# Kernel optimization log

Measured on AMD Instinct MI355X. Metric: run time of the kernel, lower is better.

The kernel has to match this reference:

```python
import jax, jax.numpy as jnp
import numpy as np

N_NODES = 50000
N_EDGES = 400000
NODE_DIM = 128
NUM_BASIS = 20
MUL0, MUL1, MUL2 = 128, 64, 32          # 128x0e + 64x1e + 32x2e
NUM_IRREPS = MUL0 + MUL1 + MUL2         # 224
SPH_DIM = MUL0 + 3 * MUL1 + 5 * MUL2    # 480
HIDDEN = NODE_DIM + NUM_IRREPS          # 352
EPS = 1e-5


def layer_norm(x, g, b):
    mu = x.mean(-1, keepdims=True)
    var = ((x - mu) ** 2).mean(-1, keepdims=True)
    return (x - mu) * jax.lax.rsqrt(var + EPS) * g + b


def o3_layer_norm(x, w, b):
    # Equivariant layer norm per irrep block (Equiformer-style, component normalization).
    s = x[:, :MUL0]                                    # l=0 scalars [N,128]
    v = x[:, MUL0:MUL0 + 3 * MUL1].reshape(-1, MUL1, 3)  # l=1 [N,64,3]
    t = x[:, MUL0 + 3 * MUL1:].reshape(-1, MUL2, 5)      # l=2 [N,32,5]
    s = s - s.mean(-1, keepdims=True)
    s = s * jax.lax.rsqrt((s ** 2).mean(-1, keepdims=True) + EPS) * w[:MUL0] + b
    nv = (v ** 2).mean(axis=(-1, -2))[:, None, None]
    v = v * jax.lax.rsqrt(nv + EPS) * w[MUL0:MUL0 + MUL1][None, :, None]
    nt = (t ** 2).mean(axis=(-1, -2))[:, None, None]
    t = t * jax.lax.rsqrt(nt + EPS) * w[MUL0 + MUL1:][None, :, None]
    return jnp.concatenate([s, v.reshape(-1, 3 * MUL1), t.reshape(-1, 5 * MUL2)], axis=-1)


def sph_harm(vec):
    # e3nn spherical harmonics (normalize=True, normalization='component') up to l=2.
    u = vec * jax.lax.rsqrt((vec ** 2).sum(-1, keepdims=True))
    x, y, z = u[:, 0], u[:, 1], u[:, 2]
    s15 = np.float32(np.sqrt(15.0))
    s5 = np.float32(np.sqrt(5.0))
    sh1 = np.float32(np.sqrt(3.0)) * u  # [E,3]
    sh2 = jnp.stack([s15 * x * z,
                     s15 * x * y,
                     s5 * (y * y - 0.5 * (x * x + z * z)),
                     s15 * y * z,
                     0.5 * s15 * (z * z - x * x)], axis=-1)  # [E,5]
    return sh1, sh2


def _forward(x_scalar, x_spherical, rbf, vec, W1, b1, W2, b2, Wrbf, ln_g, ln_b, o3_w, o3_b, edge_index):
    dst, src = edge_index[0], edge_index[1]
    scalar_in = layer_norm(x_scalar, ln_g, ln_b)          # [N,128]
    spherical_in = o3_layer_norm(x_spherical, o3_w, o3_b)  # [N,480]
    h = jax.nn.silu(scalar_in @ W1 + b1)
    scalar_out = h @ W2 + b2                               # [N,352]
    filter_weight = rbf @ Wrbf                             # [E,352]
    filter_out = scalar_out[src] * filter_weight           # gather + elementwise [E,352]
    gate = filter_out[:, :NUM_IRREPS]                      # [E,224]
    message_scalar = filter_out[:, NUM_IRREPS:]            # [E,128]
    sh1, sh2 = sph_harm(vec)
    g0 = gate[:, :MUL0]
    g1 = gate[:, MUL0:MUL0 + MUL1]
    g2 = gate[:, MUL0 + MUL1:]
    # ElementwiseTensorProduct(edge_irreps, '224x0e'): scalar gate per irrep; l=0 SH == 1.
    msg1 = (g1[:, :, None] * sh1[:, None, :]).reshape(-1, 3 * MUL1)
    msg2 = (g2[:, :, None] * sh2[:, None, :]).reshape(-1, 5 * MUL2)
    message_spherical = jnp.concatenate([g0, msg1, msg2], axis=-1)  # [E,480]
    new_scalar = scalar_in.at[dst].add(message_scalar)
    new_spherical = spherical_in.at[dst].add(message_spherical)
    return new_scalar, new_spherical


def setup_inputs() -> dict:
    key = jax.random.key(0)
    ks = jax.random.split(key, 8)
    return {
        "x_scalar": jax.random.normal(ks[0], (N_NODES, NODE_DIM), dtype=jnp.float32),
        "x_spherical": jax.random.normal(ks[1], (N_NODES, SPH_DIM), dtype=jnp.float32),
        "rbf": jax.random.normal(ks[2], (N_EDGES, NUM_BASIS), dtype=jnp.float32),
        "vec": jax.random.normal(ks[3], (N_EDGES, 3), dtype=jnp.float32),
        "W1": jax.random.normal(ks[4], (NODE_DIM, NODE_DIM), dtype=jnp.float32) * 0.05,
        "b1": jnp.zeros((NODE_DIM,), jnp.float32),
        "W2": jax.random.normal(ks[5], (NODE_DIM, HIDDEN), dtype=jnp.float32) * 0.05,
        "b2": jnp.zeros((HIDDEN,), jnp.float32),
        "Wrbf": jax.random.normal(ks[6], (NUM_BASIS, HIDDEN), dtype=jnp.float32) * 0.05,
        "ln_g": jnp.ones((NODE_DIM,), jnp.float32),
        "ln_b": jnp.zeros((NODE_DIM,), jnp.float32),
        "o3_w": jnp.ones((NUM_IRREPS,), jnp.float32),
        "o3_b": jnp.zeros((MUL0,), jnp.float32),
        "edge_index": jax.random.randint(ks[7], (2, N_EDGES), 0, N_NODES),
    }


def reference(x_scalar, x_spherical, rbf, vec, W1, b1, W2, b2, Wrbf, ln_g, ln_b, o3_w, o3_b, edge_index):
    return _forward(x_scalar, x_spherical, rbf, vec, W1, b1, W2, b2, Wrbf, ln_g, ln_b, o3_w, o3_b, edge_index)
```

## Files before the change

kernel.cpp:

```cpp
#include <hip/hip_runtime.h>
#include <hip/hip_bf16.h>

#define N_DIM   128
#define MUL0    128
#define MUL1    64
#define MUL2    32
#define NIRR    224
#define SPHD    480
#define HID     352
#define NBASIS  20
#define EPSV    1e-5f

typedef __attribute__((ext_vector_type(8))) short bf16x8;
typedef __attribute__((ext_vector_type(4))) float f32x4;

__device__ __forceinline__ float wave_sum(float v) {
  #pragma unroll
  for (int o = 32; o > 0; o >>= 1) v += __shfl_xor(v, o, 64);
  return v;
}

__device__ __forceinline__ unsigned short f2bf(float f) {
  unsigned int u = __float_as_uint(f);
  u = (u + 0x7fff + ((u >> 16) & 1)) >> 16;
  return (unsigned short)u;
}

__global__ __launch_bounds__(64) void node_norm_kernel(
    const float* __restrict__ x_scalar, const float* __restrict__ x_sph,
    const float* __restrict__ ln_g, const float* __restrict__ ln_b,
    const float* __restrict__ o3_w, const float* __restrict__ o3_b,
    float* __restrict__ out_scal, float* __restrict__ out_sph) {
  const int n = blockIdx.x;
  const int l = threadIdx.x;

  const float* xs = x_scalar + (size_t)n * N_DIM;
  float a0 = xs[l], a1 = xs[l + 64];
  float mu = wave_sum(a0 + a1) * (1.f / 128.f);
  float d0 = a0 - mu, d1 = a1 - mu;
  float var = wave_sum(d0 * d0 + d1 * d1) * (1.f / 128.f);
  float sc = rsqrtf(var + EPSV);
  float* os = out_scal + (size_t)n * N_DIM;
  os[l]      = d0 * sc * ln_g[l]      + ln_b[l];
  os[l + 64] = d1 * sc * ln_g[l + 64] + ln_b[l + 64];

  const float* xp = x_sph + (size_t)n * SPHD;
  float s0 = xp[l], s1 = xp[l + 64];
  mu = wave_sum(s0 + s1) * (1.f / 128.f);
  d0 = s0 - mu; d1 = s1 - mu;
  var = wave_sum(d0 * d0 + d1 * d1) * (1.f / 128.f);
  sc = rsqrtf(var + EPSV);
  float* op = out_sph + (size_t)n * SPHD;
  op[l]      = d0 * sc * o3_w[l]      + o3_b[l];
  op[l + 64] = d1 * sc * o3_w[l + 64] + o3_b[l + 64];

  float v0 = xp[128 + l], v1 = xp[128 + 64 + l], v2 = xp[128 + 128 + l];
  float nv = wave_sum(v0 * v0 + v1 * v1 + v2 * v2) * (1.f / 192.f);
  sc = rsqrtf(nv + EPSV);
  op[128 + l]       = v0 * sc * o3_w[MUL0 + (l) / 3];
  op[128 + 64 + l]  = v1 * sc * o3_w[MUL0 + (l + 64) / 3];
  op[128 + 128 + l] = v2 * sc * o3_w[MUL0 + (l + 128) / 3];

  float t0 = xp[320 + l], t1 = xp[320 + 64 + l];
  float t2 = (l < 32) ? xp[320 + 128 + l] : 0.f;
  float nt = wave_sum(t0 * t0 + t1 * t1 + t2 * t2) * (1.f / 160.f);
  sc = rsqrtf(nt + EPSV);
  op[320 + l]      = t0 * sc * o3_w[MUL0 + MUL1 + (l) / 5];
  op[320 + 64 + l] = t1 * sc * o3_w[MUL0 + MUL1 + (l + 64) / 5];
  if (l < 32) op[320 + 128 + l] = t2 * sc * o3_w[MUL0 + MUL1 + (l + 128) / 5];
}

__global__ void pack_b_kernel(const float* __restrict__ B, unsigned short* __restrict__ Bp,
                              int N, int NT) {
  int id = blockIdx.x * 256 + threadIdx.x;
  int total = 4 * NT * 64;
  if (id >= total) return;
  int lane = id & 63;
  int tmp = id >> 6;
  int nt = tmp % NT, ks = tmp / NT;
  int n = nt * 16 + (lane & 15);
  int kb = ks * 32 + (lane >> 4) * 8;
  unsigned short* o = Bp + (size_t)id * 8;
  #pragma unroll
  for (int j = 0; j < 8; ++j)
    o[j] = (n < N) ? f2bf(B[(size_t)(kb + j) * N + n]) : (unsigned short)0;
}

template <bool A_BF16, bool SILU, bool OUT_BF16>
__global__ __launch_bounds__(256) void mfma_gemm_kernel(
    const void* __restrict__ Ap, const unsigned short* __restrict__ Bp,
    const float* __restrict__ bias, void* __restrict__ Cp,
    int M, int N, int NT) {
  const int lane = threadIdx.x & 63;
  const int wave = threadIdx.x >> 6;
  const int bm = blockIdx.x * 64 + wave * 16;
  const int bn = blockIdx.y * 64;
  const int q = lane >> 4;
  const int arow = min(bm + (lane & 15), M - 1);

  f32x4 acc[4] = {};
  #pragma unroll
  for (int ks = 0; ks < 4; ++ks) {
    const int k = ks * 32 + q * 8;
    bf16x8 a;
    if (A_BF16) {
      a = *(const bf16x8*)((const unsigned short*)Ap + (size_t)arow * 128 + k);
    } else {
      const float* ap = (const float*)Ap + (size_t)arow * 128 + k;
      float4 f0 = *(const float4*)ap;
      float4 f1 = *(const float4*)(ap + 4);
      union { bf16x8 v; unsigned short s[8]; } cv;
      cv.s[0] = f2bf(f0.x); cv.s[1] = f2bf(f0.y); cv.s[2] = f2bf(f0.z); cv.s[3] = f2bf(f0.w);
      cv.s[4] = f2bf(f1.x); cv.s[5] = f2bf(f1.y); cv.s[6] = f2bf(f1.z); cv.s[7] = f2bf(f1.w);
      a = cv.v;
    }
    #pragma unroll
    for (int nt = 0; nt < 4; ++nt) {
      bf16x8 b = *(const bf16x8*)(Bp + ((size_t)(ks * NT + blockIdx.y * 4 + nt) * 64 + lane) * 8);
      acc[nt] = __builtin_amdgcn_mfma_f32_16x16x32_bf16(a, b, acc[nt], 0, 0, 0);
    }
  }
  #pragma unroll
  for (int nt = 0; nt < 4; ++nt) {
    int col = bn + nt * 16 + (lane & 15);
    if (col >= N) continue;
    float bz = bias[col];
    #pragma unroll
    for (int i = 0; i < 4; ++i) {
      int r = bm + q * 4 + i;
      if (r >= M) continue;
      float v = acc[nt][i] + bz;
      if (SILU) v = v / (1.f + __expf(-v));
      if (OUT_BF16) ((unsigned short*)Cp)[(size_t)r * N + col] = f2bf(v);
      else          ((float*)Cp)[(size_t)r * N + col] = v;
    }
  }
}

__global__ void hist_kernel(const int* __restrict__ ei, int* __restrict__ deg, int n_edges) {
  int e = blockIdx.x * blockDim.x + threadIdx.x;
  if (e < n_edges) atomicAdd(&deg[ei[e]], 1);
}

__global__ __launch_bounds__(1024) void scan_part_kernel(
    const int* __restrict__ deg, int* __restrict__ offs, int* __restrict__ bsum, int n) {
  __shared__ int wsum[16];
  const int tid = threadIdx.x, lane = tid & 63, wid = tid >> 6;
  int i = blockIdx.x * 1024 + tid;
  int v = (i < n) ? deg[i] : 0;
  int s = v;
  #pragma unroll
  for (int o = 1; o < 64; o <<= 1) {
    int t = __shfl_up(s, o, 64);
    if (lane >= o) s += t;
  }
  if (lane == 63) wsum[wid] = s;
  __syncthreads();
  if (wid == 0) {
    int ws = (lane < 16) ? wsum[lane] : 0;
    #pragma unroll
    for (int o = 1; o < 16; o <<= 1) {
      int t = __shfl_up(ws, o, 64);
      if (lane >= o) ws += t;
    }
    if (lane < 16) wsum[lane] = ws;
  }
  __syncthreads();
  int excl = ((wid == 0) ? 0 : wsum[wid - 1]) + s - v;
  if (i < n) offs[i] = excl;
  if (tid == 1023) bsum[blockIdx.x] = wsum[15];
}

__global__ __launch_bounds__(64) void scan_tops_kernel(
    const int* __restrict__ bsum, int* __restrict__ bbase, int* __restrict__ offs,
    int nb, int n) {
  const int lane = threadIdx.x;
  int v = (lane < nb) ? bsum[lane] : 0;
  int s = v;
  #pragma unroll
  for (int o = 1; o < 64; o <<= 1) {
    int t = __shfl_up(s, o, 64);
    if (lane >= o) s += t;
  }
  if (lane < nb) bbase[lane] = s - v;
  if (lane == 63) offs[n] = s;
}

__global__ __launch_bounds__(1024) void scan_add_kernel(
    int* __restrict__ offs, const int* __restrict__ bbase, int n) {
  int i = blockIdx.x * 1024 + threadIdx.x;
  if (i < n) offs[i] += bbase[blockIdx.x];
}

__global__ void fill_kernel(const int* __restrict__ ei, const int* __restrict__ offs,
                            int* __restrict__ cursor, int* __restrict__ sorted, int n_edges) {
  int e = blockIdx.x * blockDim.x + threadIdx.x;
  if (e < n_edges) {
    int d = ei[e];
    int p = atomicAdd(&cursor[d], 1);
    sorted[offs[d] + p] = e;
  }
}

#define NPB 8
#define S3f  1.7320508075688772f
#define S15f 3.872983346207417f
#define S5f  2.2360679774997896f

__global__ __launch_bounds__(256) void gather_kernel(
    const float* __restrict__ rbf, const float* __restrict__ vec,
    const float* __restrict__ Wrbf, const float* __restrict__ so,
    const int* __restrict__ edge_src, const int* __restrict__ offs,
    const int* __restrict__ sorted,
    float* __restrict__ out_scal, float* __restrict__ out_sph, int n_nodes) {
  const int t = threadIdx.x;
  const bool hasB = (t < 96);
  const bool needSH = (t >= 128 && t < 224);
  const int cA = t;
  const int cB = hasB ? (256 + t) : 0;

  float wA[NBASIS], wB[NBASIS];
  #pragma unroll
  for (int k = 0; k < NBASIS; ++k) {
    wA[k] = Wrbf[k * HID + cA];
    wB[k] = Wrbf[k * HID + cB];
  }

  const int nb = blockIdx.x * NPB;
  for (int nn = 0; nn < NPB; ++nn) {
    const int node = nb + nn;
    if (node >= n_nodes) break;
    float accA0 = 0.f, accA1 = 0.f, accA2 = 0.f, accA3 = 0.f, accA4 = 0.f;
    float accB = 0.f;
    const int e0 = offs[node], e1 = offs[node + 1];
    for (int ii = e0; ii < e1; ++ii) {
      const int e = sorted[ii];
      const int src = edge_src[e];

      const float4* rp = (const float4*)(rbf + (size_t)e * NBASIS);
      float4 r0 = rp[0], r1 = rp[1], r2 = rp[2], r3 = rp[3], r4 = rp[4];
      float rb[NBASIS] = {r0.x, r0.y, r0.z, r0.w, r1.x, r1.y, r1.z, r1.w,
                          r2.x, r2.y, r2.z, r2.w, r3.x, r3.y, r3.z, r3.w,
                          r4.x, r4.y, r4.z, r4.w};

      float s1x = 1.f, s1y = 1.f, s1z = 1.f, s20 = 1.f, s21 = 1.f, s22 = 1.f, s23 = 1.f, s24 = 1.f;
      if (needSH) {
        float vx = vec[3 * (size_t)e], vy = vec[3 * (size_t)e + 1], vz = vec[3 * (size_t)e + 2];
        float rn = rsqrtf(vx * vx + vy * vy + vz * vz);
        float x = vx * rn, y = vy * rn, z = vz * rn;
        s1x = S3f * x; s1y = S3f * y; s1z = S3f * z;
        s20 = S15f * x * z;
        s21 = S15f * x * y;
        s22 = S5f * (y * y - 0.5f * (x * x + z * z));
        s23 = S15f * y * z;
        s24 = 0.5f * S15f * (z * z - x * x);
      }

      float fwA = 0.f;
      #pragma unroll
      for (int k = 0; k < NBASIS; ++k) fwA += rb[k] * wA[k];
      const float* srow = so + (size_t)src * HID;
      float fA = srow[cA] * fwA;

      if (t < 128) {
        accA0 += fA;
      } else if (t < 192) {
        accA0 += fA * s1x; accA1 += fA * s1y; accA2 += fA * s1z;
      } else if (t < 224) {
        accA0 += fA * s20; accA1 += fA * s21; accA2 += fA * s22;
        accA3 += fA * s23; accA4 += fA * s24;
      } else {
        accA0 += fA;
      }

      if (hasB) {
        float fwB = 0.f;
        #pragma unroll
        for (int k = 0; k < NBASIS; ++k) fwB += rb[k] * wB[k];
        accB += srow[cB] * fwB;
      }
    }

    float* sph = out_sph + (size_t)node * SPHD;
    float* scl = out_scal + (size_t)node * N_DIM;
    if (t < 128) {
      sph[t] += accA0;
    } else if (t < 192) {
      float* p = sph + 128 + 3 * (t - 128);
      p[0] += accA0; p[1] += accA1; p[2] += accA2;
    } else if (t < 224) {
      float* p = sph + 320 + 5 * (t - 192);
      p[0] += accA0; p[1] += accA1; p[2] += accA2; p[3] += accA3; p[4] += accA4;
    } else {
      scl[t - 224] += accA0;
    }
    if (hasB) scl[t + 32] += accB;
  }
}

extern "C" void kernel_launch(void* const* d_in, const int* in_sizes, int n_in,
                              void* d_out, int out_size, void* d_ws, size_t ws_size,
                              hipStream_t stream) {
  const float* x_scalar = (const float*)d_in[0];
  const float* x_sph    = (const float*)d_in[1];
  const float* rbf      = (const float*)d_in[2];
  const float* vec      = (const float*)d_in[3];
  const float* W1       = (const float*)d_in[4];
  const float* b1       = (const float*)d_in[5];
  const float* W2       = (const float*)d_in[6];
  const float* b2       = (const float*)d_in[7];
  const float* Wrbf     = (const float*)d_in[8];
  const float* ln_g     = (const float*)d_in[9];
  const float* ln_b     = (const float*)d_in[10];
  const float* o3_w     = (const float*)d_in[11];
  const float* o3_b     = (const float*)d_in[12];
  const int*   edge_idx = (const int*)d_in[13];

  const int n_nodes = in_sizes[0] / N_DIM;
  const int n_edges = in_sizes[2] / NBASIS;

  float* out_scal = (float*)d_out;
  float* out_sph  = out_scal + (size_t)n_nodes * N_DIM;

  float*          ws_so = (float*)d_ws;
  unsigned short* h_bf  = (unsigned short*)(ws_so + (size_t)n_nodes * HID);
  unsigned short* bp1   = h_bf + (size_t)n_nodes * N_DIM;
  unsigned short* bp2   = bp1 + 16384;
  int* deg    = (int*)(bp2 + 49152);
  int* cursor = deg + n_nodes;
  int* offs   = cursor + n_nodes;
  int* bsum   = offs + n_nodes + 1;
  int* bbase  = bsum + 64;
  int* sorted = bbase + 64;

  const int* edge_dst = edge_idx;
  const int* edge_src = edge_idx + n_edges;

  node_norm_kernel<<<n_nodes, 64, 0, stream>>>(
      x_scalar, x_sph, ln_g, ln_b, o3_w, o3_b, out_scal, out_sph);

  pack_b_kernel<<<8, 256, 0, stream>>>(W1, bp1, N_DIM, 8);
  pack_b_kernel<<<24, 256, 0, stream>>>(W2, bp2, HID, 24);

  {
    dim3 g((n_nodes + 63) / 64, 2);
    mfma_gemm_kernel<false, true, true><<<g, 256, 0, stream>>>(
        out_scal, bp1, b1, h_bf, n_nodes, N_DIM, 8);
  }
  {
    dim3 g((n_nodes + 63) / 64, 6);
    mfma_gemm_kernel<true, false, false><<<g, 256, 0, stream>>>(
        h_bf, bp2, b2, ws_so, n_nodes, HID, 24);
  }

  hipMemsetAsync(deg, 0, sizeof(int) * 2 * n_nodes, stream);
  hist_kernel<<<(n_edges + 255) / 256, 256, 0, stream>>>(edge_dst, deg, n_edges);
  const int nb = (n_nodes + 1023) / 1024;
  scan_part_kernel<<<nb, 1024, 0, stream>>>(deg, offs, bsum, n_nodes);
  scan_tops_kernel<<<1, 64, 0, stream>>>(bsum, bbase, offs, nb, n_nodes);
  scan_add_kernel<<<nb, 1024, 0, stream>>>(offs, bbase, n_nodes);
  fill_kernel<<<(n_edges + 255) / 256, 256, 0, stream>>>(edge_dst, offs, cursor, sorted, n_edges);

  gather_kernel<<<(n_nodes + NPB - 1) / NPB, 256, 0, stream>>>(
      rbf, vec, Wrbf, ws_so, edge_src, offs, sorted, out_scal, out_sph, n_nodes);
}
```

Measured before the change: 691.8 us.

## Pre-permute edge data into CSR order and unroll gather loop by two

Adds a pregather kernel that copies rbf, vec and source indices into destination-sorted order, so the gather kernel reads them contiguously instead of through the sorted-index indirection. The gather loop is unrolled by two edges to overlap the source-row loads, spherical-harmonic math is computed only by the threads that need it, and nodes per block drop from 8 to 4. The node norm kernel now packs four nodes per 256-thread block. This costs an extra pass over edge data and more workspace.

```diff
diff --git a/kernel.cpp b/kernel.cpp
--- a/kernel.cpp
+++ b/kernel.cpp
@@ -26,13 +26,14 @@
   return (unsigned short)u;
 }
 
-__global__ __launch_bounds__(64) void node_norm_kernel(
+__global__ __launch_bounds__(256) void node_norm_kernel(
     const float* __restrict__ x_scalar, const float* __restrict__ x_sph,
     const float* __restrict__ ln_g, const float* __restrict__ ln_b,
     const float* __restrict__ o3_w, const float* __restrict__ o3_b,
-    float* __restrict__ out_scal, float* __restrict__ out_sph) {
-  const int n = blockIdx.x;
-  const int l = threadIdx.x;
+    float* __restrict__ out_scal, float* __restrict__ out_sph, int n_nodes) {
+  const int n = blockIdx.x * 4 + (threadIdx.x >> 6);
+  if (n >= n_nodes) return;
+  const int l = threadIdx.x & 63;
 
   const float* xs = x_scalar + (size_t)n * N_DIM;
   float a0 = xs[l], a1 = xs[l + 64];
@@ -202,22 +203,85 @@
   }
 }
 
-#define NPB 8
+__global__ __launch_bounds__(256) void pregather_kernel(
+    const float* __restrict__ rbf, const float* __restrict__ vec,
+    const int* __restrict__ edge_src, const int* __restrict__ sorted,
+    float* __restrict__ rbf_s, float* __restrict__ vec_s, int* __restrict__ src_s,
+    int n_edges) {
+  const int i = blockIdx.x * 256 + threadIdx.x;
+  const int nf4 = n_edges * 5;
+  if (i < nf4) {
+    int ii = i / 5, j = i - ii * 5;
+    int e = sorted[ii];
+    ((float4*)rbf_s)[i] = ((const float4*)rbf)[(size_t)e * 5 + j];
+  }
+  const int nv = n_edges * 3;
+  if (i < nv) {
+    int ii = i / 3, j = i - ii * 3;
+    int e = sorted[ii];
+    vec_s[i] = vec[(size_t)e * 3 + j];
+  }
+  if (i < n_edges) {
+    src_s[i] = edge_src[sorted[i]];
+  }
+}
+
+#define NPB 4
 #define S3f  1.7320508075688772f
 #define S15f 3.872983346207417f
 #define S5f  2.2360679774997896f
 
+__device__ __forceinline__ void edge_accum(
+    int ii, float sA, float sB,
+    const float* __restrict__ rbf_s, const float* __restrict__ vec_s,
+    const float* wA, const float* wB, int t, bool hasB,
+    float& a0, float& a1, float& a2, float& a3, float& a4, float& aB) {
+  const float4* rp = (const float4*)(rbf_s + (size_t)ii * NBASIS);
+  float4 r0 = rp[0], r1 = rp[1], r2 = rp[2], r3 = rp[3], r4 = rp[4];
+  float rb[NBASIS] = {r0.x, r0.y, r0.z, r0.w, r1.x, r1.y, r1.z, r1.w,
+                      r2.x, r2.y, r2.z, r2.w, r3.x, r3.y, r3.z, r3.w,
+                      r4.x, r4.y, r4.z, r4.w};
+  float fwA = 0.f;
+  #pragma unroll
+  for (int k = 0; k < NBASIS; ++k) fwA += rb[k] * wA[k];
+  float fA = sA * fwA;
+
+  if (t < 128) {
+    a0 += fA;
+  } else if (t < 224) {
+    float vx = vec_s[3 * (size_t)ii], vy = vec_s[3 * (size_t)ii + 1], vz = vec_s[3 * (size_t)ii + 2];
+    float rn = rsqrtf(vx * vx + vy * vy + vz * vz);
+    float x = vx * rn, y = vy * rn, z = vz * rn;
+    if (t < 192) {
+      a0 += fA * (S3f * x); a1 += fA * (S3f * y); a2 += fA * (S3f * z);
+    } else {
+      a0 += fA * (S15f * x * z);
+      a1 += fA * (S15f * x * y);
+      a2 += fA * (S5f * (y * y - 0.5f * (x * x + z * z)));
+      a3 += fA * (S15f * y * z);
+      a4 += fA * (0.5f * S15f * (z * z - x * x));
+    }
+  } else {
+    a0 += fA;
+  }
+
+  if (hasB) {
+    float fwB = 0.f;
+    #pragma unroll
+    for (int k = 0; k < NBASIS; ++k) fwB += rb[k] * wB[k];
+    aB += sB * fwB;
+  }
+}
+
 __global__ __launch_bounds__(256) void gather_kernel(
-    const float* __restrict__ rbf, const float* __restrict__ vec,
+    const float* __restrict__ rbf_s, const float* __restrict__ vec_s,
     const float* __restrict__ Wrbf, const float* __restrict__ so,
-    const int* __restrict__ edge_src, const int* __restrict__ offs,
-    const int* __restrict__ sorted,
+    const int* __restrict__ src_s, const int* __restrict__ offs,
     float* __restrict__ out_scal, float* __restrict__ out_sph, int n_nodes) {
   const int t = threadIdx.x;
   const bool hasB = (t < 96);
-  const bool needSH = (t >= 128 && t < 224);
   const int cA = t;
-  const int cB = hasB ? (256 + t) : 0;
+  const int cB = hasB ? (256 + t) : 256;
 
   float wA[NBASIS], wB[NBASIS];
   #pragma unroll
@@ -233,52 +297,27 @@
     float accA0 = 0.f, accA1 = 0.f, accA2 = 0.f, accA3 = 0.f, accA4 = 0.f;
     float accB = 0.f;
     const int e0 = offs[node], e1 = offs[node + 1];
-    for (int ii = e0; ii < e1; ++ii) {
-      const int e = sorted[ii];
-      const int src = edge_src[e];
-
-      const float4* rp = (const float4*)(rbf + (size_t)e * NBASIS);
-      float4 r0 = rp[0], r1 = rp[1], r2 = rp[2], r3 = rp[3], r4 = rp[4];
-      float rb[NBASIS] = {r0.x, r0.y, r0.z, r0.w, r1.x, r1.y, r1.z, r1.w,
-                          r2.x, r2.y, r2.z, r2.w, r3.x, r3.y, r3.z, r3.w,
-                          r4.x, r4.y, r4.z, r4.w};
-
-      float s1x = 1.f, s1y = 1.f, s1z = 1.f, s20 = 1.f, s21 = 1.f, s22 = 1.f, s23 = 1.f, s24 = 1.f;
-      if (needSH) {
-        float vx = vec[3 * (size_t)e], vy = vec[3 * (size_t)e + 1], vz = vec[3 * (size_t)e + 2];
-        float rn = rsqrtf(vx * vx + vy * vy + vz * vz);
-        float x = vx * rn, y = vy * rn, z = vz * rn;
-        s1x = S3f * x; s1y = S3f * y; s1z = S3f * z;
-        s20 = S15f * x * z;
-        s21 = S15f * x * y;
-        s22 = S5f * (y * y - 0.5f * (x * x + z * z));
-        s23 = S15f * y * z;
-        s24 = 0.5f * S15f * (z * z - x * x);
-      }
-
-      float fwA = 0.f;
-      #pragma unroll
-      for (int k = 0; k < NBASIS; ++k) fwA += rb[k] * wA[k];
-      const float* srow = so + (size_t)src * HID;
-      float fA = srow[cA] * fwA;
-
-      if (t < 128) {
-        accA0 += fA;
-      } else if (t < 192) {
-        accA0 += fA * s1x; accA1 += fA * s1y; accA2 += fA * s1z;
-      } else if (t < 224) {
-        accA0 += fA * s20; accA1 += fA * s21; accA2 += fA * s22;
-        accA3 += fA * s23; accA4 += fA * s24;
-      } else {
-        accA0 += fA;
-      }
-
-      if (hasB) {
-        float fwB = 0.f;
-        #pragma unroll
-        for (int k = 0; k < NBASIS; ++k) fwB += rb[k] * wB[k];
-        accB += srow[cB] * fwB;
-      }
+
+    int ii = e0;
+    for (; ii + 2 <= e1; ii += 2) {
+      const int s0 = src_s[ii], s1 = src_s[ii + 1];
+      const float* p0 = so + (size_t)s0 * HID;
+      const float* p1 = so + (size_t)s1 * HID;
+      float sA0 = p0[cA], sA1 = p1[cA];
+      float sB0 = hasB ? p0[cB] : 0.f;
+      float sB1 = hasB ? p1[cB] : 0.f;
+      edge_accum(ii,     sA0, sB0, rbf_s, vec_s, wA, wB, t, hasB,
+                 accA0, accA1, accA2, accA3, accA4, accB);
+      edge_accum(ii + 1, sA1, sB1, rbf_s, vec_s, wA, wB, t, hasB,
+                 accA0, accA1, accA2, accA3, accA4, accB);
+    }
+    if (ii < e1) {
+      const int s0 = src_s[ii];
+      const float* p0 = so + (size_t)s0 * HID;
+      float sA0 = p0[cA];
+      float sB0 = hasB ? p0[cB] : 0.f;
+      edge_accum(ii, sA0, sB0, rbf_s, vec_s, wA, wB, t, hasB,
+                 accA0, accA1, accA2, accA3, accA4, accB);
     }
 
     float* sph = out_sph + (size_t)node * SPHD;
@@ -322,10 +361,13 @@
   float* out_scal = (float*)d_out;
   float* out_sph  = out_scal + (size_t)n_nodes * N_DIM;
 
-  float*          ws_so = (float*)d_ws;
-  unsigned short* h_bf  = (unsigned short*)(ws_so + (size_t)n_nodes * HID);
-  unsigned short* bp1   = h_bf + (size_t)n_nodes * N_DIM;
-  unsigned short* bp2   = bp1 + 16384;
+  float* rbf_s = (float*)d_ws;
+  float* vec_s = rbf_s + (size_t)n_edges * NBASIS;
+  int*   src_s = (int*)(vec_s + (size_t)n_edges * 3);
+  float* ws_so = (float*)(src_s + n_edges);
+  unsigned short* h_bf = (unsigned short*)(ws_so + (size_t)n_nodes * HID);
+  unsigned short* bp1  = h_bf + (size_t)n_nodes * N_DIM;
+  unsigned short* bp2  = bp1 + 16384;
   int* deg    = (int*)(bp2 + 49152);
   int* cursor = deg + n_nodes;
   int* offs   = cursor + n_nodes;
@@ -336,8 +378,8 @@
   const int* edge_dst = edge_idx;
   const int* edge_src = edge_idx + n_edges;
 
-  node_norm_kernel<<<n_nodes, 64, 0, stream>>>(
-      x_scalar, x_sph, ln_g, ln_b, o3_w, o3_b, out_scal, out_sph);
+  node_norm_kernel<<<(n_nodes + 3) / 4, 256, 0, stream>>>(
+      x_scalar, x_sph, ln_g, ln_b, o3_w, o3_b, out_scal, out_sph, n_nodes);
 
   pack_b_kernel<<<8, 256, 0, stream>>>(W1, bp1, N_DIM, 8);
   pack_b_kernel<<<24, 256, 0, stream>>>(W2, bp2, HID, 24);
@@ -361,6 +403,9 @@
   scan_add_kernel<<<nb, 1024, 0, stream>>>(offs, bbase, n_nodes);
   fill_kernel<<<(n_edges + 255) / 256, 256, 0, stream>>>(edge_dst, offs, cursor, sorted, n_edges);
 
+  pregather_kernel<<<(n_edges * 5 + 255) / 256, 256, 0, stream>>>(
+      rbf, vec, edge_src, sorted, rbf_s, vec_s, src_s, n_edges);
+
   gather_kernel<<<(n_nodes + NPB - 1) / NPB, 256, 0, stream>>>(
-      rbf, vec, Wrbf, ws_so, edge_src, offs, sorted, out_scal, out_sph, n_nodes);
-}
+      rbf_s, vec_s, Wrbf, ws_so, src_s, offs, out_scal, out_sph, n_nodes);
+}
```

Result: faster. 668.9 us (-3.3%).
